# Kernel optimization log

Measured on AMD Instinct MI355X. Metric: run time of the kernel, lower is better.

Reference implementation:

```python
import jax, jax.numpy as jnp
import numpy as np

V, E, H = 32000, 128, 256
B, S, T = 32, 128, 128


def lstm(emb, Wih, Whh, bih, bhh, h0, c0):
    """Single-layer batch_first LSTM matching torch.nn.LSTM (gate order i,f,g,o).
    emb: [B,T,E] -> (outputs [B,T,H], h_T [B,H], c_T [B,H])."""
    b = bih + bhh  # [4H]
    xg = jnp.einsum('bte,ge->btg', emb, Wih) + b  # precompute input gates [B,T,4H]

    def step(carry, xg_t):
        h, c = carry
        gates = xg_t + h @ Whh.T  # [B,4H]
        i, f, g, o = jnp.split(gates, 4, axis=-1)
        i, f, o = jax.nn.sigmoid(i), jax.nn.sigmoid(f), jax.nn.sigmoid(o)
        g = jnp.tanh(g)
        c = f * c + i * g
        h = o * jnp.tanh(c)
        return (h, c), h

    (hT, cT), hs = jax.lax.scan(step, (h0, c0), jnp.swapaxes(xg, 0, 1))
    return jnp.swapaxes(hs, 0, 1), hT, cT


def setup_inputs() -> dict:
    key = jax.random.key(0)
    ks = jax.random.split(key, 14)
    s_e, s_h = 1.0 / np.sqrt(H), 1.0 / np.sqrt(H)
    return {
        'x': jax.random.randint(ks[0], (B, S), 0, V),
        'y': jax.random.randint(ks[1], (B, T), 0, V),
        'enc_emb': jax.random.normal(ks[2], (V, E), jnp.float32),
        'dec_emb': jax.random.normal(ks[3], (V, E), jnp.float32),
        'Wih_enc': jax.random.uniform(ks[4], (4 * H, E), jnp.float32, -s_e, s_e),
        'Whh_enc': jax.random.uniform(ks[5], (4 * H, H), jnp.float32, -s_h, s_h),
        'bih_enc': jax.random.uniform(ks[6], (4 * H,), jnp.float32, -s_h, s_h),
        'bhh_enc': jax.random.uniform(ks[7], (4 * H,), jnp.float32, -s_h, s_h),
        'Wih_dec': jax.random.uniform(ks[8], (4 * H, E), jnp.float32, -s_e, s_e),
        'Whh_dec': jax.random.uniform(ks[9], (4 * H, H), jnp.float32, -s_h, s_h),
        'bih_dec': jax.random.uniform(ks[10], (4 * H,), jnp.float32, -s_h, s_h),
        'bhh_dec': jax.random.uniform(ks[11], (4 * H,), jnp.float32, -s_h, s_h),
        'W_out': jax.random.uniform(ks[12], (V, H), jnp.float32, -s_h, s_h),
        'b_out': jax.random.uniform(ks[13], (V,), jnp.float32, -s_h, s_h),
    }


def reference(x, y, enc_emb, dec_emb, Wih_enc, Whh_enc, bih_enc, bhh_enc,
              Wih_dec, Whh_dec, bih_dec, bhh_dec, W_out, b_out):
    h0 = jnp.zeros((x.shape[0], H), jnp.float32)
    c0 = jnp.zeros((x.shape[0], H), jnp.float32)
    # encoder
    x_emb = enc_emb[x]  # [B,S,E]
    _, h, c = lstm(x_emb, Wih_enc, Whh_enc, bih_enc, bhh_enc, h0, c0)
    # decoder (teacher forcing)
    y_emb = dec_emb[y]  # [B,T,E]
    dec_out, _, _ = lstm(y_emb, Wih_dec, Whh_dec, bih_dec, bhh_dec, h, c)
    logits = jnp.einsum('bth,vh->btv', dec_out, W_out) + b_out  # [B,T,V]
    return logits
```

## Files before the change

### kernel.cpp

```cpp
#include <hip/hip_runtime.h>


typedef _Float16 half2v __attribute__((ext_vector_type(2)));
typedef short bf16x8 __attribute__((ext_vector_type(8)));
typedef float f32x4 __attribute__((ext_vector_type(4)));

__device__ __forceinline__ unsigned short f2h_bits(float f) {
  _Float16 h = (_Float16)f;
  return __builtin_bit_cast(unsigned short, h);
}

__device__ __forceinline__ unsigned short f2bf_bits(float f) {
  unsigned u = __builtin_bit_cast(unsigned, f);
  u += 0x7fffu + ((u >> 16) & 1u);
  return (unsigned short)(u >> 16);
}

__device__ __forceinline__ float fdot2u(unsigned wu, unsigned hu, float acc) {
#if defined(__has_builtin) && __has_builtin(__builtin_amdgcn_fdot2)
  return __builtin_amdgcn_fdot2(__builtin_bit_cast(half2v, wu),
                                __builtin_bit_cast(half2v, hu), acc, false);
#else
  half2v a = __builtin_bit_cast(half2v, wu);
  half2v b = __builtin_bit_cast(half2v, hu);
  return acc + (float)a[0] * (float)b[0] + (float)a[1] * (float)b[1];
#endif
}

__device__ __forceinline__ float tanh_fast(float x) {
  float e = __expf(2.f * x);
  return 1.f - 2.f / (e + 1.f);
}

__device__ __forceinline__ float sigmoid_fast(float x) {
  return 1.f / (1.f + __expf(-x));
}

__device__ __forceinline__ void gload_lds16(const void* g, void* l) {
#if defined(__has_builtin) && __has_builtin(__builtin_amdgcn_global_load_lds)
  __builtin_amdgcn_global_load_lds(
      (const __attribute__((address_space(1))) void*)g,
      (__attribute__((address_space(3))) void*)l, 16, 0, 0);
#else
  *(uint4*)l = *(const uint4*)g;
#endif
}

__global__ void prep_kernel(const float* __restrict__ WhhE, const float* __restrict__ WhhD,
                            const float* __restrict__ Wout,
                            unsigned* __restrict__ WhhP, unsigned short* __restrict__ WoutB) {
  int i = blockIdx.x * blockDim.x + threadIdx.x;
  int stride = gridDim.x * blockDim.x;
  for (int idx = i; idx < 262144; idx += stride) {
    int p = idx >> 17;
    int rem = idx & 131071;
    int d = rem >> 10;
    int g = rem & 1023;
    const float* W = p ? WhhD : WhhE;
    float a = W[g * 256 + 2 * d];
    float b = W[g * 256 + 2 * d + 1];
    WhhP[idx] = (unsigned)f2h_bits(a) | ((unsigned)f2h_bits(b) << 16);
  }
  for (int idx = i; idx < 8192000; idx += stride) {
    WoutB[idx] = f2bf_bits(Wout[idx]);
  }
}

__global__ __launch_bounds__(256, 2) void xg_kernel(
    const int* __restrict__ x, const int* __restrict__ y,
    const float* __restrict__ enc_emb, const float* __restrict__ dec_emb,
    const float* __restrict__ Wih_enc, const float* __restrict__ Wih_dec,
    float* __restrict__ xg) {
  __shared__ float Al[64][132];
  __shared__ float Bl[64][132];
  __shared__ int tok[64];
  const int nb = blockIdx.x;
  const int mbb = blockIdx.y;
  const int m0 = mbb * 64;
  const int p = mbb >> 6;
  const int tid = threadIdx.x;

  if (tid < 64) {
    int mloc = (m0 + tid) & 4095;
    tok[tid] = p ? y[mloc] : x[mloc];
  }
  __syncthreads();

  const float* emb = p ? dec_emb : enc_emb;
  const float* Wih = p ? Wih_dec : Wih_enc;
  {
    int ri = tid & 63, seg = tid >> 6;
    const float* er = emb + (size_t)tok[ri] * 128 + seg * 32;
    const float* wr = Wih + (size_t)(nb * 64 + ri) * 128 + seg * 32;
#pragma unroll
    for (int c = 0; c < 8; ++c) {
      *(float4*)&Al[ri][seg * 32 + c * 4] = *(const float4*)&er[c * 4];
      *(float4*)&Bl[ri][seg * 32 + c * 4] = *(const float4*)&wr[c * 4];
    }
  }
  __syncthreads();

  const int tx = tid & 15, ty = tid >> 4;
  float acc[4][4];
#pragma unroll
  for (int mm = 0; mm < 4; ++mm)
#pragma unroll
    for (int nn = 0; nn < 4; ++nn) acc[mm][nn] = 0.f;

  for (int k4 = 0; k4 < 32; ++k4) {
    float4 av[4], bv[4];
#pragma unroll
    for (int mm = 0; mm < 4; ++mm) av[mm] = *(const float4*)&Al[mm * 16 + ty][k4 * 4];
#pragma unroll
    for (int nn = 0; nn < 4; ++nn) bv[nn] = *(const float4*)&Bl[nn * 16 + tx][k4 * 4];
#pragma unroll
    for (int mm = 0; mm < 4; ++mm)
#pragma unroll
      for (int nn = 0; nn < 4; ++nn) {
        acc[mm][nn] = fmaf(av[mm].x, bv[nn].x, acc[mm][nn]);
        acc[mm][nn] = fmaf(av[mm].y, bv[nn].y, acc[mm][nn]);
        acc[mm][nn] = fmaf(av[mm].z, bv[nn].z, acc[mm][nn]);
        acc[mm][nn] = fmaf(av[mm].w, bv[nn].w, acc[mm][nn]);
      }
  }
#pragma unroll
  for (int mm = 0; mm < 4; ++mm)
#pragma unroll
    for (int nn = 0; nn < 4; ++nn)
      xg[(size_t)(m0 + mm * 16 + ty) * 1024 + nb * 64 + nn * 16 + tx] = acc[mm][nn];
}

__global__ __launch_bounds__(1024, 1) void lstm_kernel(
    const float* __restrict__ xg, const unsigned* __restrict__ WhhP,
    const float* __restrict__ bih_enc, const float* __restrict__ bhh_enc,
    const float* __restrict__ bih_dec, const float* __restrict__ bhh_dec,
    unsigned short* __restrict__ decO) {
  const int b = blockIdx.x;
  const int t = threadIdx.x;
  const int g = t;
  const int q = t >> 8;
  const int j = t & 255;

  __shared__ __align__(16) unsigned h2[128];
  __shared__ float gact[4][256];
  __shared__ unsigned WL[18 * 2048];

  if (t < 128) h2[t] = 0u;
  float c_r = 0.f;
  __syncthreads();

  unsigned wqd[92];
  float bias_g = 0.f;

  float xgv_n = xg[(size_t)(b << 7) * 1024 + g];

  for (int s = 0; s < 256; ++s) {
    const int p = s >> 7;
    const int tt = s & 127;

    if ((s & 127) == 0) {
      const unsigned* base = WhhP + (p << 17);
#pragma unroll
      for (int d = 0; d < 92; ++d) wqd[d] = base[(d << 10) + g];
#pragma unroll
      for (int dd = 0; dd < 36; ++dd)
        WL[((dd >> 1) << 11) + (g << 1) + (dd & 1)] = base[((92 + dd) << 10) + g];
      bias_g = p ? (bih_dec[g] + bhh_dec[g]) : (bih_enc[g] + bhh_enc[g]);
    }

    const float xgv = xgv_n;
    if (s < 255) {
      const int sn = s + 1;
      xgv_n = xg[(size_t)(((sn >> 7) << 12) + (b << 7) + (sn & 127)) * 1024 + g];
    }

    float a0 = 0.f, a1 = 0.f, a2 = 0.f, a3 = 0.f;
#pragma unroll
    for (int c = 0; c < 23; ++c) {
      const uint4 hv = *(const uint4*)&h2[c << 2];
      a0 = fdot2u(wqd[4 * c + 0], hv.x, a0);
      a1 = fdot2u(wqd[4 * c + 1], hv.y, a1);
      a2 = fdot2u(wqd[4 * c + 2], hv.z, a2);
      a3 = fdot2u(wqd[4 * c + 3], hv.w, a3);
    }
#pragma unroll
    for (int c = 23; c < 32; ++c) {
      const uint4 hv = *(const uint4*)&h2[c << 2];
      const int dp0 = (4 * c - 92) >> 1;
      const uint2 w01 = *(const uint2*)&WL[(dp0 << 11) + (g << 1)];
      const uint2 w23 = *(const uint2*)&WL[((dp0 + 1) << 11) + (g << 1)];
      a0 = fdot2u(w01.x, hv.x, a0);
      a1 = fdot2u(w01.y, hv.y, a1);
      a2 = fdot2u(w23.x, hv.z, a2);
      a3 = fdot2u(w23.y, hv.w, a3);
    }
    const float accf = bias_g + xgv + ((a0 + a1) + (a2 + a3));

    const float act = (q == 2) ? tanh_fast(accf) : sigmoid_fast(accf);
    gact[q][j] = act;
    __syncthreads();

    if (t < 256) {
      const float iv = gact[0][t];
      const float fv = gact[1][t];
      const float gv = gact[2][t];
      const float ov = gact[3][t];
      c_r = fv * c_r + iv * gv;
      const float hh = ov * tanh_fast(c_r);
      if (p) decO[(size_t)((b << 7) + tt) * 256 + t] = f2bf_bits(hh);
      const float hn = __shfl_down(hh, 1, 64);
      if (!(t & 1))
        h2[t >> 1] = (unsigned)f2h_bits(hh) | ((unsigned)f2h_bits(hn) << 16);
    }
    __syncthreads();
  }
}

__global__ __launch_bounds__(256, 2) void proj_kernel(
    const unsigned short* __restrict__ A,
    const unsigned short* __restrict__ Bw,
    const float* __restrict__ bias, float* __restrict__ out) {
  __shared__ unsigned short Al[128 * 128];
  __shared__ unsigned short Bl[128 * 128];
  const int mb = blockIdx.x;
  const int nb = blockIdx.y;
  const int tid = threadIdx.x;
  const int wv = tid >> 6, ln = tid & 63;
  const int wm = wv & 1, wn = wv >> 1;
  const int l16 = ln & 15, lq = ln >> 4;

  f32x4 acc[4][4] = {};

  for (int kc = 0; kc < 2; ++kc) {
#pragma unroll
    for (int it = 0; it < 8; ++it) {
      int st = it * 256 + tid;
      int m = st >> 4, k8 = st & 15;
      const unsigned short* gp =
          A + (size_t)(mb * 128 + m) * 256 + kc * 128 + ((k8 ^ (m & 15)) << 3);
      gload_lds16(gp, &Al[st << 3]);
    }
#pragma unroll
    for (int it = 0; it < 8; ++it) {
      int st = it * 256 + tid;
      int m = st >> 4, k8 = st & 15;
      const unsigned short* gp =
          Bw + (size_t)(nb * 128 + m) * 256 + kc * 128 + ((k8 ^ (m & 15)) << 3);
      gload_lds16(gp, &Bl[st << 3]);
    }
    asm volatile("s_waitcnt vmcnt(0)" ::: "memory");
    __syncthreads();

#pragma unroll
    for (int ks = 0; ks < 4; ++ks) {
      const int k8 = (ks << 2) + lq;
      bf16x8 af[4], bf[4];
#pragma unroll
      for (int mt = 0; mt < 4; ++mt) {
        int m = (wm << 6) + (mt << 4) + l16;
        af[mt] = *(const bf16x8*)&Al[(m << 7) + ((k8 ^ (m & 15)) << 3)];
      }
#pragma unroll
      for (int nt = 0; nt < 4; ++nt) {
        int n = (wn << 6) + (nt << 4) + l16;
        bf[nt] = *(const bf16x8*)&Bl[(n << 7) + ((k8 ^ (n & 15)) << 3)];
      }
#pragma unroll
      for (int mt = 0; mt < 4; ++mt)
#pragma unroll
        for (int nt = 0; nt < 4; ++nt)
          acc[mt][nt] = __builtin_amdgcn_mfma_f32_16x16x32_bf16(af[mt], bf[nt],
                                                                acc[mt][nt], 0, 0, 0);
    }
    __syncthreads();
  }

#pragma unroll
  for (int nt = 0; nt < 4; ++nt) {
    const int gcol = nb * 128 + (wn << 6) + (nt << 4) + l16;
    const float bs = bias[gcol];
#pragma unroll
    for (int mt = 0; mt < 4; ++mt) {
      const int grow0 = mb * 128 + (wm << 6) + (mt << 4) + (lq << 2);
#pragma unroll
      for (int rr = 0; rr < 4; ++rr)
        out[(size_t)(grow0 + rr) * 32000 + gcol] = acc[mt][nt][rr] + bs;
    }
  }
}

extern "C" void kernel_launch(void* const* d_in, const int* in_sizes, int n_in,
                              void* d_out, int out_size, void* d_ws, size_t ws_size,
                              hipStream_t stream) {
  const int* x = (const int*)d_in[0];
  const int* y = (const int*)d_in[1];
  const float* enc_emb = (const float*)d_in[2];
  const float* dec_emb = (const float*)d_in[3];
  const float* Wih_enc = (const float*)d_in[4];
  const float* Whh_enc = (const float*)d_in[5];
  const float* bih_enc = (const float*)d_in[6];
  const float* bhh_enc = (const float*)d_in[7];
  const float* Wih_dec = (const float*)d_in[8];
  const float* Whh_dec = (const float*)d_in[9];
  const float* bih_dec = (const float*)d_in[10];
  const float* bhh_dec = (const float*)d_in[11];
  const float* W_out = (const float*)d_in[12];
  const float* b_out = (const float*)d_in[13];

  char* ws = (char*)d_ws;
  float* xg = (float*)ws;
  unsigned* WhhP = (unsigned*)(ws + 33554432);
  unsigned short* WoutB = (unsigned short*)(ws + 34603008);
  unsigned short* decO = (unsigned short*)(ws + 50987008);
  if (ws_size < 57344000) return;

  prep_kernel<<<4096, 256, 0, stream>>>(Whh_enc, Whh_dec, W_out, WhhP, WoutB);
  xg_kernel<<<dim3(16, 128), 256, 0, stream>>>(x, y, enc_emb, dec_emb, Wih_enc, Wih_dec, xg);
  lstm_kernel<<<32, 1024, 0, stream>>>(xg, WhhP, bih_enc, bhh_enc, bih_dec, bhh_dec, decO);
  proj_kernel<<<dim3(32, 250), 256, 0, stream>>>(decO, WoutB, b_out, (float*)d_out);
}
```

Measured before the change: 1.278 ms.

## Halve LSTM block size so each thread computes two gate rows

The recurrent LSTM kernel now launches 512 threads per batch element instead of 1024. Each thread owns two gate rows (g and g+512), holding two register-resident weight slices and a uint4-packed LDS tail. The aim is to reuse each h vector load across two dot products and to cut barrier participants. The cost is doubled register pressure (184 weight registers plus accumulators), which risks spilling, and each thread now does twice the serial work per timestep.

```diff
diff --git a/kernel.cpp b/kernel.cpp
--- a/kernel.cpp
+++ b/kernel.cpp
@@ -130,74 +130,104 @@
       xg[(size_t)(m0 + mm * 16 + ty) * 1024 + nb * 64 + nn * 16 + tx] = acc[mm][nn];
 }
 
-__global__ __launch_bounds__(1024, 1) void lstm_kernel(
+__global__ __launch_bounds__(512, 2) void lstm_kernel(
     const float* __restrict__ xg, const unsigned* __restrict__ WhhP,
     const float* __restrict__ bih_enc, const float* __restrict__ bhh_enc,
     const float* __restrict__ bih_dec, const float* __restrict__ bhh_dec,
     unsigned short* __restrict__ decO) {
   const int b = blockIdx.x;
   const int t = threadIdx.x;
-  const int g = t;
-  const int q = t >> 8;
+  const int g0 = t;
+  const int g1 = t + 512;
+  const int q0 = t >> 8;
   const int j = t & 255;
 
   __shared__ __align__(16) unsigned h2[128];
   __shared__ float gact[4][256];
-  __shared__ unsigned WL[18 * 2048];
+  __shared__ __align__(16) unsigned WL[9 * 1024 * 4];
 
   if (t < 128) h2[t] = 0u;
   float c_r = 0.f;
   __syncthreads();
 
-  unsigned wqd[92];
-  float bias_g = 0.f;
-
-  float xgv_n = xg[(size_t)(b << 7) * 1024 + g];
+  unsigned w0[92], w1[92];
+  float bias0 = 0.f, bias1 = 0.f;
+
+  const float* xp = xg + (size_t)(b << 7) * 1024;
+  float xv0 = xp[g0];
+  float xv1 = xp[g1];
 
   for (int s = 0; s < 256; ++s) {
     const int p = s >> 7;
     const int tt = s & 127;
 
-    if ((s & 127) == 0) {
+    if (tt == 0) {
       const unsigned* base = WhhP + (p << 17);
 #pragma unroll
-      for (int d = 0; d < 92; ++d) wqd[d] = base[(d << 10) + g];
-#pragma unroll
-      for (int dd = 0; dd < 36; ++dd)
-        WL[((dd >> 1) << 11) + (g << 1) + (dd & 1)] = base[((92 + dd) << 10) + g];
-      bias_g = p ? (bih_dec[g] + bhh_dec[g]) : (bih_enc[g] + bhh_enc[g]);
-    }
-
-    const float xgv = xgv_n;
+      for (int d = 0; d < 92; ++d) {
+        w0[d] = base[(d << 10) + g0];
+        w1[d] = base[(d << 10) + g1];
+      }
+#pragma unroll
+      for (int cc = 0; cc < 9; ++cc) {
+        uint4 qa, qb;
+        qa.x = base[((92 + 4 * cc + 0) << 10) + g0];
+        qa.y = base[((92 + 4 * cc + 1) << 10) + g0];
+        qa.z = base[((92 + 4 * cc + 2) << 10) + g0];
+        qa.w = base[((92 + 4 * cc + 3) << 10) + g0];
+        qb.x = base[((92 + 4 * cc + 0) << 10) + g1];
+        qb.y = base[((92 + 4 * cc + 1) << 10) + g1];
+        qb.z = base[((92 + 4 * cc + 2) << 10) + g1];
+        qb.w = base[((92 + 4 * cc + 3) << 10) + g1];
+        *(uint4*)&WL[((cc << 10) + g0) << 2] = qa;
+        *(uint4*)&WL[((cc << 10) + g1) << 2] = qb;
+      }
+      bias0 = p ? (bih_dec[g0] + bhh_dec[g0]) : (bih_enc[g0] + bhh_enc[g0]);
+      bias1 = p ? (bih_dec[g1] + bhh_dec[g1]) : (bih_enc[g1] + bhh_enc[g1]);
+    }
+
+    const float x0 = xv0, x1 = xv1;
     if (s < 255) {
-      const int sn = s + 1;
-      xgv_n = xg[(size_t)(((sn >> 7) << 12) + (b << 7) + (sn & 127)) * 1024 + g];
-    }
-
-    float a0 = 0.f, a1 = 0.f, a2 = 0.f, a3 = 0.f;
+      xp += (tt == 127) ? 3969 * 1024 : 1024;
+      xv0 = xp[g0];
+      xv1 = xp[g1];
+    }
+
+    float a00 = 0.f, a01 = 0.f, a02 = 0.f, a03 = 0.f;
+    float a10 = 0.f, a11 = 0.f, a12 = 0.f, a13 = 0.f;
 #pragma unroll
     for (int c = 0; c < 23; ++c) {
       const uint4 hv = *(const uint4*)&h2[c << 2];
-      a0 = fdot2u(wqd[4 * c + 0], hv.x, a0);
-      a1 = fdot2u(wqd[4 * c + 1], hv.y, a1);
-      a2 = fdot2u(wqd[4 * c + 2], hv.z, a2);
-      a3 = fdot2u(wqd[4 * c + 3], hv.w, a3);
+      a00 = fdot2u(w0[4 * c + 0], hv.x, a00);
+      a01 = fdot2u(w0[4 * c + 1], hv.y, a01);
+      a02 = fdot2u(w0[4 * c + 2], hv.z, a02);
+      a03 = fdot2u(w0[4 * c + 3], hv.w, a03);
+      a10 = fdot2u(w1[4 * c + 0], hv.x, a10);
+      a11 = fdot2u(w1[4 * c + 1], hv.y, a11);
+      a12 = fdot2u(w1[4 * c + 2], hv.z, a12);
+      a13 = fdot2u(w1[4 * c + 3], hv.w, a13);
     }
 #pragma unroll
     for (int c = 23; c < 32; ++c) {
       const uint4 hv = *(const uint4*)&h2[c << 2];
-      const int dp0 = (4 * c - 92) >> 1;
-      const uint2 w01 = *(const uint2*)&WL[(dp0 << 11) + (g << 1)];
-      const uint2 w23 = *(const uint2*)&WL[((dp0 + 1) << 11) + (g << 1)];
-      a0 = fdot2u(w01.x, hv.x, a0);
-      a1 = fdot2u(w01.y, hv.y, a1);
-      a2 = fdot2u(w23.x, hv.z, a2);
-      a3 = fdot2u(w23.y, hv.w, a3);
-    }
-    const float accf = bias_g + xgv + ((a0 + a1) + (a2 + a3));
-
-    const float act = (q == 2) ? tanh_fast(accf) : sigmoid_fast(accf);
-    gact[q][j] = act;
+      const uint4 qa = *(const uint4*)&WL[(((c - 23) << 10) + g0) << 2];
+      const uint4 qb = *(const uint4*)&WL[(((c - 23) << 10) + g1) << 2];
+      a00 = fdot2u(qa.x, hv.x, a00);
+      a01 = fdot2u(qa.y, hv.y, a01);
+      a02 = fdot2u(qa.z, hv.z, a02);
+      a03 = fdot2u(qa.w, hv.w, a03);
+      a10 = fdot2u(qb.x, hv.x, a10);
+      a11 = fdot2u(qb.y, hv.y, a11);
+      a12 = fdot2u(qb.z, hv.z, a12);
+      a13 = fdot2u(qb.w, hv.w, a13);
+    }
+    const float acc0 = bias0 + x0 + ((a00 + a01) + (a02 + a03));
+    const float acc1 = bias1 + x1 + ((a10 + a11) + (a12 + a13));
+
+    const float act0 = sigmoid_fast(acc0);
+    const float act1 = (q0 == 0) ? tanh_fast(acc1) : sigmoid_fast(acc1);
+    gact[q0][j] = act0;
+    gact[q0 + 2][j] = act1;
     __syncthreads();
 
     if (t < 256) {
@@ -316,6 +346,6 @@
 
   prep_kernel<<<4096, 256, 0, stream>>>(Whh_enc, Whh_dec, W_out, WhhP, WoutB);
   xg_kernel<<<dim3(16, 128), 256, 0, stream>>>(x, y, enc_emb, dec_emb, Wih_enc, Wih_dec, xg);
-  lstm_kernel<<<32, 1024, 0, stream>>>(xg, WhhP, bih_enc, bhh_enc, bih_dec, bhh_dec, decO);
+  lstm_kernel<<<32, 512, 0, stream>>>(xg, WhhP, bih_enc, bhh_enc, bih_dec, bhh_dec, decO);
   proj_kernel<<<dim3(32, 250), 256, 0, stream>>>(decO, WoutB, b_out, (float*)d_out);
 }
```

Result: slower. 3.057 ms (+139.2%).

## Keep W_out tile resident in registers and stream A rows with double buffering

Applied to the files above, without the earlier changes.

The projection GEMM now gives each block a 64-column slice of W_out, which it loads once into LDS and then into registers for the full K=256. It then loops over all 4096 rows in 32-row chunks, double-buffering the A chunks through LDS with async loads so the next chunk arrives while the current one is computed and stored. The aim is to cut repeated B-tile loads and per-block setup, and to overlap loads with output stores. In exchange the grid shrinks to 500 long-running blocks, each with only a small MFMA tile per iteration, which may limit latency hiding and leave occupancy uneven across CUs.

```diff
diff --git a/kernel.cpp b/kernel.cpp
--- a/kernel.cpp
+++ b/kernel.cpp
@@ -220,72 +220,74 @@
     const unsigned short* __restrict__ A,
     const unsigned short* __restrict__ Bw,
     const float* __restrict__ bias, float* __restrict__ out) {
-  __shared__ unsigned short Al[128 * 128];
-  __shared__ unsigned short Bl[128 * 128];
-  const int mb = blockIdx.x;
-  const int nb = blockIdx.y;
+  __shared__ unsigned short Bl[64 * 256];
+  __shared__ unsigned short Al[2][32 * 256];
+  const int n0 = blockIdx.x << 6;
   const int tid = threadIdx.x;
   const int wv = tid >> 6, ln = tid & 63;
-  const int wm = wv & 1, wn = wv >> 1;
+  const int wm = wv & 1;
+  const int wn = wv >> 1;
   const int l16 = ln & 15, lq = ln >> 4;
 
-  f32x4 acc[4][4] = {};
-
-  for (int kc = 0; kc < 2; ++kc) {
-#pragma unroll
-    for (int it = 0; it < 8; ++it) {
-      int st = it * 256 + tid;
-      int m = st >> 4, k8 = st & 15;
-      const unsigned short* gp =
-          A + (size_t)(mb * 128 + m) * 256 + kc * 128 + ((k8 ^ (m & 15)) << 3);
-      gload_lds16(gp, &Al[st << 3]);
-    }
-#pragma unroll
-    for (int it = 0; it < 8; ++it) {
-      int st = it * 256 + tid;
-      int m = st >> 4, k8 = st & 15;
-      const unsigned short* gp =
-          Bw + (size_t)(nb * 128 + m) * 256 + kc * 128 + ((k8 ^ (m & 15)) << 3);
-      gload_lds16(gp, &Bl[st << 3]);
-    }
-    asm volatile("s_waitcnt vmcnt(0)" ::: "memory");
+#pragma unroll
+  for (int it = 0; it < 8; ++it) {
+    int st = it * 256 + tid;
+    int m = st >> 5, k8 = st & 31;
+    gload_lds16(Bw + (size_t)(n0 + m) * 256 + ((k8 ^ (m & 15)) << 3), &Bl[st << 3]);
+  }
+#pragma unroll
+  for (int it = 0; it < 4; ++it) {
+    int st = it * 256 + tid;
+    int m = st >> 5, k8 = st & 31;
+    gload_lds16(A + (size_t)m * 256 + ((k8 ^ (m & 15)) << 3), &Al[0][st << 3]);
+  }
+  asm volatile("s_waitcnt vmcnt(0)" ::: "memory");
+  __syncthreads();
+
+  bf16x8 bfr[2][8];
+#pragma unroll
+  for (int nt = 0; nt < 2; ++nt)
+#pragma unroll
+    for (int ks = 0; ks < 8; ++ks) {
+      int n = (wn << 5) + (nt << 4) + l16;
+      int k8 = (ks << 2) + lq;
+      bfr[nt][ks] = *(const bf16x8*)&Bl[((n << 5) | (k8 ^ (n & 15))) << 3];
+    }
+  const int gc0 = n0 + (wn << 5) + l16;
+  const float bs0 = bias[gc0];
+  const float bs1 = bias[gc0 + 16];
+
+  for (int c = 0; c < 128; ++c) {
+    const int cur = c & 1;
+    if (c < 127) {
+      const unsigned short* Ab = A + (size_t)(c + 1) * (32 * 256);
+#pragma unroll
+      for (int it = 0; it < 4; ++it) {
+        int st = it * 256 + tid;
+        int m = st >> 5, k8 = st & 31;
+        gload_lds16(Ab + (size_t)m * 256 + ((k8 ^ (m & 15)) << 3), &Al[cur ^ 1][st << 3]);
+      }
+    }
+
+    f32x4 acc0 = {}, acc1 = {};
+#pragma unroll
+    for (int ks = 0; ks < 8; ++ks) {
+      const int k8 = (ks << 2) + lq;
+      const int m = (wm << 4) + l16;
+      const bf16x8 af = *(const bf16x8*)&Al[cur][((m << 5) | (k8 ^ (m & 15))) << 3];
+      acc0 = __builtin_amdgcn_mfma_f32_16x16x32_bf16(af, bfr[0][ks], acc0, 0, 0, 0);
+      acc1 = __builtin_amdgcn_mfma_f32_16x16x32_bf16(af, bfr[1][ks], acc1, 0, 0, 0);
+    }
+
+    const int grow0 = (c << 5) + (wm << 4) + (lq << 2);
+#pragma unroll
+    for (int rr = 0; rr < 4; ++rr) {
+      out[(size_t)(grow0 + rr) * 32000 + gc0] = acc0[rr] + bs0;
+      out[(size_t)(grow0 + rr) * 32000 + gc0 + 16] = acc1[rr] + bs1;
+    }
+
+    asm volatile("s_waitcnt vmcnt(8)" ::: "memory");
     __syncthreads();
-
-#pragma unroll
-    for (int ks = 0; ks < 4; ++ks) {
-      const int k8 = (ks << 2) + lq;
-      bf16x8 af[4], bf[4];
-#pragma unroll
-      for (int mt = 0; mt < 4; ++mt) {
-        int m = (wm << 6) + (mt << 4) + l16;
-        af[mt] = *(const bf16x8*)&Al[(m << 7) + ((k8 ^ (m & 15)) << 3)];
-      }
-#pragma unroll
-      for (int nt = 0; nt < 4; ++nt) {
-        int n = (wn << 6) + (nt << 4) + l16;
-        bf[nt] = *(const bf16x8*)&Bl[(n << 7) + ((k8 ^ (n & 15)) << 3)];
-      }
-#pragma unroll
-      for (int mt = 0; mt < 4; ++mt)
-#pragma unroll
-        for (int nt = 0; nt < 4; ++nt)
-          acc[mt][nt] = __builtin_amdgcn_mfma_f32_16x16x32_bf16(af[mt], bf[nt],
-                                                                acc[mt][nt], 0, 0, 0);
-    }
-    __syncthreads();
-  }
-
-#pragma unroll
-  for (int nt = 0; nt < 4; ++nt) {
-    const int gcol = nb * 128 + (wn << 6) + (nt << 4) + l16;
-    const float bs = bias[gcol];
-#pragma unroll
-    for (int mt = 0; mt < 4; ++mt) {
-      const int grow0 = mb * 128 + (wm << 6) + (mt << 4) + (lq << 2);
-#pragma unroll
-      for (int rr = 0; rr < 4; ++rr)
-        out[(size_t)(grow0 + rr) * 32000 + gcol] = acc[mt][nt][rr] + bs;
-    }
   }
 }
 
@@ -317,5 +319,5 @@
   prep_kernel<<<4096, 256, 0, stream>>>(Whh_enc, Whh_dec, W_out, WhhP, WoutB);
   xg_kernel<<<dim3(16, 128), 256, 0, stream>>>(x, y, enc_emb, dec_emb, Wih_enc, Wih_dec, xg);
   lstm_kernel<<<32, 1024, 0, stream>>>(xg, WhhP, bih_enc, bhh_enc, bih_dec, bhh_dec, decO);
-  proj_kernel<<<dim3(32, 250), 256, 0, stream>>>(decO, WoutB, b_out, (float*)d_out);
-}
+  proj_kernel<<<500, 256, 0, stream>>>(decO, WoutB, b_out, (float*)d_out);
+}
```

Result: no change. 1.282 ms (+0.3%).
